# Optimization experiments

Measured on AMD Instinct MI355X. Metric: run time of the kernel, lower is better.

## Reference

```python
import jax, jax.numpy as jnp
import numpy as np

N_NODES = 2097152  # total nodes
HIDDEN = 64        # feature dim D

def setup_inputs() -> dict:
    key = jax.random.key(0)
    features = jax.random.normal(key, (N_NODES, HIDDEN), dtype=jnp.float32)
    return {"features": features, "n_per_graph": 512}

def reference(features, n_per_graph):
    # features: [N, D]; N = B * n_per_graph (uniform segments)
    N, D = features.shape
    B = N // n_per_graph
    X = features.reshape(B, n_per_graph, D)          # [B, n, D]
    mu = jnp.mean(X, axis=1, keepdims=True)          # [B, 1, D]
    Xc = X - mu                                      # mean-centered
    # per-graph covariance: (Xc^T Xc) / n  -> [B, D, D]
    cov = jnp.einsum('bnd,bne->bde', Xc, Xc) / jnp.asarray(n_per_graph, X.dtype)
    iu0, iu1 = jnp.triu_indices(D)                   # upper triangle incl. diag
    return cov[:, iu0, iu1]                          # [B, D*(D+1)/2]
```

## Files before the change

### kernel.cpp

```cpp
#include <hip/hip_runtime.h>
#include <hip/hip_bf16.h>


#define DD   64
#define NPG  512
#define NCH  16

typedef __bf16 bf16x8 __attribute__((ext_vector_type(8)));
typedef float  f32x4  __attribute__((ext_vector_type(4)));

typedef __attribute__((address_space(3))) void       lds_void;
typedef const __attribute__((address_space(1))) void gbl_void;

#define MFMA(a, b, c) __builtin_amdgcn_mfma_f32_16x16x32_bf16((a), (b), (c), 0, 0, 0)
#define AUX_NT 2

__global__ __launch_bounds__(256, 4)
void cov_pool_kernel(const float* __restrict__ X, float* __restrict__ out) {
  __shared__ __align__(16) float sh[4][2048];
  __shared__ float muv[DD];

  const int tid  = threadIdx.x;
  const int lane = tid & 63;
  const int w    = tid >> 6;
  const int q    = lane & 15;
  const int grp  = lane >> 4;
  const long g   = blockIdx.x;
  const float* Xg = X + g * (long)(NPG * DD);

  const float* srcA = Xg + (size_t)((2 * w) * 4 + grp) * DD + 4 * (q ^ (2 * w));

  const int vb0 = grp * 512 + (( 0 | q) ^ (8 * grp));
  const int vb1 = grp * 512 + ((16 | q) ^ (8 * grp));
  const int vb2 = grp * 512 + ((32 | q) ^ (8 * grp));
  const int vb3 = grp * 512 + ((48 | q) ^ (8 * grp));

  f32x4 z = {0.f, 0.f, 0.f, 0.f};
  f32x4 a00=z,a01=z,a02=z,a03=z,a11=z,a12=z,a13=z,a22=z,a23=z,a33=z;
  f32x4 am0=z,am1=z,am2=z,am3=z;

  bf16x8 ones;
  #pragma unroll
  for (int j = 0; j < 8; ++j) ones[j] = (__bf16)1.0f;

  auto stage = [&](int c) {
    const float* s = srcA + (size_t)c * (32 * DD);
    float* d = &sh[c & 3][(2 * w) * 256];
    __builtin_amdgcn_global_load_lds((gbl_void*)s,         (lds_void*)d,         16, 0, AUX_NT);
    __builtin_amdgcn_global_load_lds((gbl_void*)(s + 256), (lds_void*)(d + 256), 16, 0, AUX_NT);
  };

  stage(0); stage(1); stage(2);

  #pragma unroll
  for (int c = 0; c < NCH; ++c) {
    asm volatile("s_waitcnt lgkmcnt(0)" ::: "memory");
    if (c < NCH - 2)       asm volatile("s_waitcnt vmcnt(4)" ::: "memory");
    else if (c == NCH - 2) asm volatile("s_waitcnt vmcnt(2)" ::: "memory");
    else                   asm volatile("s_waitcnt vmcnt(0)" ::: "memory");
    __builtin_amdgcn_s_barrier();
    asm volatile("" ::: "memory");

    if (c + 3 < NCH) stage(c + 3);

    const float* buf = sh[c & 3];
    bf16x8 b0, b1, b2, b3;
    #pragma unroll
    for (int j = 0; j < 8; ++j) {
      b0[j] = (__bf16)buf[vb0 + 64 * j];
      b1[j] = (__bf16)buf[vb1 + 64 * j];
      b2[j] = (__bf16)buf[vb2 + 64 * j];
      b3[j] = (__bf16)buf[vb3 + 64 * j];
    }
    if (w == 0)      { a00 = MFMA(b0, b0, a00); a01 = MFMA(b0, b1, a01); a02 = MFMA(b0, b2, a02); }
    else if (w == 1) { a03 = MFMA(b0, b3, a03); a11 = MFMA(b1, b1, a11); a12 = MFMA(b1, b2, a12); }
    else if (w == 2) { a13 = MFMA(b1, b3, a13); a22 = MFMA(b2, b2, a22); a23 = MFMA(b2, b3, a23); }
    else             { a33 = MFMA(b3, b3, a33);
                       am0 = MFMA(ones, b0, am0); am1 = MFMA(ones, b1, am1);
                       am2 = MFMA(ones, b2, am2); am3 = MFMA(ones, b3, am3); }
  }

  if (w == 3 && lane < 16) {
    const float inv_n = 1.f / NPG;
    muv[ 0 + lane] = am0[0] * inv_n;
    muv[16 + lane] = am1[0] * inv_n;
    muv[32 + lane] = am2[0] * inv_n;
    muv[48 + lane] = am3[0] * inv_n;
  }
  asm volatile("s_waitcnt lgkmcnt(0)" ::: "memory");
  __builtin_amdgcn_s_barrier();
  asm volatile("" ::: "memory");

  const float inv_n = 1.f / NPG;
  float* og = out + g * 2080L;
  const int rl4 = grp * 4;
  auto wtile = [&](int tr, int tc, const f32x4& A, bool diag) {
    const int j = tc * 16 + q;
    const float mcj = muv[j];
    #pragma unroll
    for (int r = 0; r < 4; ++r) {
      const int i = tr * 16 + rl4 + r;
      if (!diag || j >= i)
        og[i * DD - (i * (i - 1)) / 2 + (j - i)] = A[r] * inv_n - muv[i] * mcj;
    }
  };
  if (w == 0)      { wtile(0, 0, a00, true);  wtile(0, 1, a01, false); wtile(0, 2, a02, false); }
  else if (w == 1) { wtile(0, 3, a03, false); wtile(1, 1, a11, true);  wtile(1, 2, a12, false); }
  else if (w == 2) { wtile(1, 3, a13, false); wtile(2, 2, a22, true);  wtile(2, 3, a23, false); }
  else             { wtile(3, 3, a33, true); }
}

extern "C" void kernel_launch(void* const* d_in, const int* in_sizes, int n_in,
                              void* d_out, int out_size, void* d_ws, size_t ws_size,
                              hipStream_t stream) {
  const float* X = (const float*)d_in[0];
  float* out = (float*)d_out;
  const int N = in_sizes[0] / DD;
  const int B = N / NPG;
  cov_pool_kernel<<<dim3(B), dim3(256), 0, stream>>>(X, out);
}
```

Measured before the change: 106.6 us.

## Process four graphs per block with a prefetch pipeline that runs across graphs

Each block now loops over up to four consecutive graphs instead of one, and the grid shrinks to a quarter of its former size. The three-deep global-to-LDS prefetch ring keeps going across graph boundaries, so the next graph's first chunks load while the current graph's results are written. This removes per-block launch and pipeline fill/drain costs, and lets the output stores overlap with loads. In exchange the grid becomes smaller and less able to balance load if residency is uneven, and the wait-count logic now depends on a runtime chunk total.

```diff
diff --git a/kernel.cpp b/kernel.cpp
--- a/kernel.cpp
+++ b/kernel.cpp
@@ -5,6 +5,7 @@
 #define DD   64
 #define NPG  512
 #define NCH  16
+#define GPB  4
 
 typedef __bf16 bf16x8 __attribute__((ext_vector_type(8)));
 typedef float  f32x4  __attribute__((ext_vector_type(4)));
@@ -16,7 +17,8 @@
 #define AUX_NT 2
 
 __global__ __launch_bounds__(256, 4)
-void cov_pool_kernel(const float* __restrict__ X, float* __restrict__ out) {
+void cov_pool_kernel(const float* __restrict__ X, float* __restrict__ out,
+                     int n_graphs) {
   __shared__ __align__(16) float sh[4][2048];
   __shared__ float muv[DD];
 
@@ -25,89 +27,94 @@
   const int w    = tid >> 6;
   const int q    = lane & 15;
   const int grp  = lane >> 4;
-  const long g   = blockIdx.x;
-  const float* Xg = X + g * (long)(NPG * DD);
+  const long g0  = (long)blockIdx.x * GPB;
+  const int ngr  = (n_graphs - g0 < GPB) ? (int)(n_graphs - g0) : GPB;
+  const int T    = ngr * NCH;
 
-  const float* srcA = Xg + (size_t)((2 * w) * 4 + grp) * DD + 4 * (q ^ (2 * w));
+  const float* srcA = X + g0 * (NPG * DD)
+                    + (size_t)((2 * w) * 4 + grp) * DD + 4 * (q ^ (2 * w));
 
   const int vb0 = grp * 512 + (( 0 | q) ^ (8 * grp));
   const int vb1 = grp * 512 + ((16 | q) ^ (8 * grp));
   const int vb2 = grp * 512 + ((32 | q) ^ (8 * grp));
   const int vb3 = grp * 512 + ((48 | q) ^ (8 * grp));
 
-  f32x4 z = {0.f, 0.f, 0.f, 0.f};
-  f32x4 a00=z,a01=z,a02=z,a03=z,a11=z,a12=z,a13=z,a22=z,a23=z,a33=z;
-  f32x4 am0=z,am1=z,am2=z,am3=z;
-
   bf16x8 ones;
   #pragma unroll
   for (int j = 0; j < 8; ++j) ones[j] = (__bf16)1.0f;
 
-  auto stage = [&](int c) {
-    const float* s = srcA + (size_t)c * (32 * DD);
-    float* d = &sh[c & 3][(2 * w) * 256];
+  auto stage = [&](int cc) {
+    const float* s = srcA + (size_t)cc * (32 * DD);
+    float* d = &sh[cc & 3][(2 * w) * 256];
     __builtin_amdgcn_global_load_lds((gbl_void*)s,         (lds_void*)d,         16, 0, AUX_NT);
     __builtin_amdgcn_global_load_lds((gbl_void*)(s + 256), (lds_void*)(d + 256), 16, 0, AUX_NT);
   };
 
   stage(0); stage(1); stage(2);
 
-  #pragma unroll
-  for (int c = 0; c < NCH; ++c) {
+  const float inv_n = 1.f / NPG;
+  int cc = 0;
+  #pragma unroll 1
+  for (int gi = 0; gi < ngr; ++gi) {
+    f32x4 z = {0.f, 0.f, 0.f, 0.f};
+    f32x4 a00=z,a01=z,a02=z,a03=z,a11=z,a12=z,a13=z,a22=z,a23=z,a33=z;
+    f32x4 am0=z,am1=z,am2=z,am3=z;
+
+    #pragma unroll
+    for (int c = 0; c < NCH; ++c, ++cc) {
+      asm volatile("s_waitcnt lgkmcnt(0)" ::: "memory");
+      if (cc < T - 2)       asm volatile("s_waitcnt vmcnt(4)" ::: "memory");
+      else if (cc == T - 2) asm volatile("s_waitcnt vmcnt(2)" ::: "memory");
+      else                  asm volatile("s_waitcnt vmcnt(0)" ::: "memory");
+      __builtin_amdgcn_s_barrier();
+      asm volatile("" ::: "memory");
+
+      if (cc + 3 < T) stage(cc + 3);
+
+      const float* buf = sh[cc & 3];
+      bf16x8 b0, b1, b2, b3;
+      #pragma unroll
+      for (int j = 0; j < 8; ++j) {
+        b0[j] = (__bf16)buf[vb0 + 64 * j];
+        b1[j] = (__bf16)buf[vb1 + 64 * j];
+        b2[j] = (__bf16)buf[vb2 + 64 * j];
+        b3[j] = (__bf16)buf[vb3 + 64 * j];
+      }
+      if (w == 0)      { a00 = MFMA(b0, b0, a00); a01 = MFMA(b0, b1, a01); a02 = MFMA(b0, b2, a02); }
+      else if (w == 1) { a03 = MFMA(b0, b3, a03); a11 = MFMA(b1, b1, a11); a12 = MFMA(b1, b2, a12); }
+      else if (w == 2) { a13 = MFMA(b1, b3, a13); a22 = MFMA(b2, b2, a22); a23 = MFMA(b2, b3, a23); }
+      else             { a33 = MFMA(b3, b3, a33);
+                         am0 = MFMA(ones, b0, am0); am1 = MFMA(ones, b1, am1);
+                         am2 = MFMA(ones, b2, am2); am3 = MFMA(ones, b3, am3); }
+    }
+
+    if (w == 3 && lane < 16) {
+      muv[ 0 + lane] = am0[0] * inv_n;
+      muv[16 + lane] = am1[0] * inv_n;
+      muv[32 + lane] = am2[0] * inv_n;
+      muv[48 + lane] = am3[0] * inv_n;
+    }
     asm volatile("s_waitcnt lgkmcnt(0)" ::: "memory");
-    if (c < NCH - 2)       asm volatile("s_waitcnt vmcnt(4)" ::: "memory");
-    else if (c == NCH - 2) asm volatile("s_waitcnt vmcnt(2)" ::: "memory");
-    else                   asm volatile("s_waitcnt vmcnt(0)" ::: "memory");
     __builtin_amdgcn_s_barrier();
     asm volatile("" ::: "memory");
 
-    if (c + 3 < NCH) stage(c + 3);
-
-    const float* buf = sh[c & 3];
-    bf16x8 b0, b1, b2, b3;
-    #pragma unroll
-    for (int j = 0; j < 8; ++j) {
-      b0[j] = (__bf16)buf[vb0 + 64 * j];
-      b1[j] = (__bf16)buf[vb1 + 64 * j];
-      b2[j] = (__bf16)buf[vb2 + 64 * j];
-      b3[j] = (__bf16)buf[vb3 + 64 * j];
-    }
-    if (w == 0)      { a00 = MFMA(b0, b0, a00); a01 = MFMA(b0, b1, a01); a02 = MFMA(b0, b2, a02); }
-    else if (w == 1) { a03 = MFMA(b0, b3, a03); a11 = MFMA(b1, b1, a11); a12 = MFMA(b1, b2, a12); }
-    else if (w == 2) { a13 = MFMA(b1, b3, a13); a22 = MFMA(b2, b2, a22); a23 = MFMA(b2, b3, a23); }
-    else             { a33 = MFMA(b3, b3, a33);
-                       am0 = MFMA(ones, b0, am0); am1 = MFMA(ones, b1, am1);
-                       am2 = MFMA(ones, b2, am2); am3 = MFMA(ones, b3, am3); }
+    float* og = out + (g0 + gi) * 2080L;
+    const int rl4 = grp * 4;
+    auto wtile = [&](int tr, int tc, const f32x4& A, bool diag) {
+      const int j = tc * 16 + q;
+      const float mcj = muv[j];
+      #pragma unroll
+      for (int r = 0; r < 4; ++r) {
+        const int i = tr * 16 + rl4 + r;
+        if (!diag || j >= i)
+          og[i * DD - (i * (i - 1)) / 2 + (j - i)] = A[r] * inv_n - muv[i] * mcj;
+      }
+    };
+    if (w == 0)      { wtile(0, 0, a00, true);  wtile(0, 1, a01, false); wtile(0, 2, a02, false); }
+    else if (w == 1) { wtile(0, 3, a03, false); wtile(1, 1, a11, true);  wtile(1, 2, a12, false); }
+    else if (w == 2) { wtile(1, 3, a13, false); wtile(2, 2, a22, true);  wtile(2, 3, a23, false); }
+    else             { wtile(3, 3, a33, true); }
   }
-
-  if (w == 3 && lane < 16) {
-    const float inv_n = 1.f / NPG;
-    muv[ 0 + lane] = am0[0] * inv_n;
-    muv[16 + lane] = am1[0] * inv_n;
-    muv[32 + lane] = am2[0] * inv_n;
-    muv[48 + lane] = am3[0] * inv_n;
-  }
-  asm volatile("s_waitcnt lgkmcnt(0)" ::: "memory");
-  __builtin_amdgcn_s_barrier();
-  asm volatile("" ::: "memory");
-
-  const float inv_n = 1.f / NPG;
-  float* og = out + g * 2080L;
-  const int rl4 = grp * 4;
-  auto wtile = [&](int tr, int tc, const f32x4& A, bool diag) {
-    const int j = tc * 16 + q;
-    const float mcj = muv[j];
-    #pragma unroll
-    for (int r = 0; r < 4; ++r) {
-      const int i = tr * 16 + rl4 + r;
-      if (!diag || j >= i)
-        og[i * DD - (i * (i - 1)) / 2 + (j - i)] = A[r] * inv_n - muv[i] * mcj;
-    }
-  };
-  if (w == 0)      { wtile(0, 0, a00, true);  wtile(0, 1, a01, false); wtile(0, 2, a02, false); }
-  else if (w == 1) { wtile(0, 3, a03, false); wtile(1, 1, a11, true);  wtile(1, 2, a12, false); }
-  else if (w == 2) { wtile(1, 3, a13, false); wtile(2, 2, a22, true);  wtile(2, 3, a23, false); }
-  else             { wtile(3, 3, a33, true); }
 }
 
 extern "C" void kernel_launch(void* const* d_in, const int* in_sizes, int n_in,
@@ -117,5 +124,5 @@
   float* out = (float*)d_out;
   const int N = in_sizes[0] / DD;
   const int B = N / NPG;
-  cov_pool_kernel<<<dim3(B), dim3(256), 0, stream>>>(X, out);
+  cov_pool_kernel<<<dim3((B + GPB - 1) / GPB), dim3(256), 0, stream>>>(X, out, B);
 }
```

Result: slower. 123.5 us (+15.9%).
